# Kernel optimization log

Hardware: AMD Instinct MI355X
Metric: run time of the kernel (lower is better)

Reference implementation:

```python
import jax, jax.numpy as jnp
import numpy as np

N_CLASSES = 18
NMS_PRE = 1000   # test_cfg.nms_pre, per level
K_NMS = 500      # per-class candidates entering greedy NMS
SCORE_THR = 0.01
IOU_THR = 0.5
LEVEL_NS = [600000, 300000, 150000, 75000]


def _decode(points, pred):
    # fcaf3d axis-aligned decode: pred = (dx-, dx+, dy-, dy+, dz-, dz+) >= 0
    cx = points[:, 0] + (pred[:, 1] - pred[:, 0]) / 2
    cy = points[:, 1] + (pred[:, 3] - pred[:, 2]) / 2
    cz = points[:, 2] + (pred[:, 5] - pred[:, 4]) / 2
    w = pred[:, 0] + pred[:, 1]
    l = pred[:, 2] + pred[:, 3]
    h = pred[:, 4] + pred[:, 5]
    return jnp.stack([cx, cy, cz, w, l, h], axis=-1)  # [N, 6]


def _iou3d(b):
    # axis-aligned 3D IoU, b: [K,6] (cx,cy,cz,w,l,h) -> [K,K]
    mn = b[:, :3] - b[:, 3:] / 2
    mx = b[:, :3] + b[:, 3:] / 2
    lt = jnp.maximum(mn[:, None, :], mn[None, :, :])
    rb = jnp.minimum(mx[:, None, :], mx[None, :, :])
    inter = jnp.clip(rb - lt, 0.0).prod(-1)
    vol = jnp.clip(mx - mn, 0.0).prod(-1)
    return inter / (vol[:, None] + vol[None, :] - inter + 1e-6)


def _level(centerness, bbox_pred, cls_score, points):
    # fused score: cls.sigmoid() * centerness.sigmoid()
    scores = jax.nn.sigmoid(cls_score) * jax.nn.sigmoid(centerness)  # [N,C]
    max_scores = scores.max(axis=1)
    _, ids = jax.lax.top_k(max_scores, NMS_PRE)  # per-level prefilter
    bboxes = _decode(points[ids], bbox_pred[ids])  # [NMS_PRE, 6]
    return bboxes, scores[ids]


def _nms_class(boxes, scores):
    # boxes [M,6], scores [M] for one class -> greedy NMS on top K_NMS
    valid = scores > SCORE_THR
    s = jnp.where(valid, scores, -1.0)
    sv, order = jax.lax.top_k(s, K_NMS)  # sorted desc
    b = boxes[order]
    v = sv > SCORE_THR
    iou = _iou3d(b)  # [K,K]
    idx = jnp.arange(K_NMS)

    def body(i, sup):
        alive = jnp.logical_not(sup[i])
        return sup | (alive & (iou[i] > IOU_THR) & (idx > i))

    sup = jax.lax.fori_loop(0, K_NMS, body, jnp.logical_not(v))
    keep = jnp.logical_not(sup) & v
    return b, sv, keep


def _forward(levels):
    mlvl_bboxes, mlvl_scores = [], []
    for (cn, bp, cs, pt) in levels:
        b, s = _level(cn, bp, cs, pt)
        mlvl_bboxes.append(b)
        mlvl_scores.append(s)
    bboxes = jnp.concatenate(mlvl_bboxes)  # [4*NMS_PRE, 6]
    scores = jnp.concatenate(mlvl_scores)  # [4*NMS_PRE, C]
    # per-class NMS (vmap over class dim)
    b, sv, keep = jax.vmap(_nms_class, in_axes=(None, 1))(bboxes, scores)
    labels = jnp.broadcast_to(jnp.arange(N_CLASSES, dtype=jnp.int32)[:, None], sv.shape)
    return (b.reshape(-1, 6), sv.reshape(-1), labels.reshape(-1), keep.reshape(-1))


def setup_inputs() -> dict:
    key = jax.random.key(0)
    out = {}
    for li, n in enumerate(LEVEL_NS):
        k1, k2, k3, k4, key = jax.random.split(key, 5)
        out[f'centerness{li}'] = jax.random.normal(k1, (n, 1), jnp.float32)
        out[f'bbox_pred{li}'] = jax.random.uniform(k2, (n, 6), jnp.float32)  # non-negative distances
        out[f'cls_score{li}'] = jax.random.normal(k3, (n, N_CLASSES), jnp.float32)
        out[f'points{li}'] = jax.random.normal(k4, (n, 3), jnp.float32) * 2.0
    return out


def reference(centerness0, bbox_pred0, cls_score0, points0,
              centerness1, bbox_pred1, cls_score1, points1,
              centerness2, bbox_pred2, cls_score2, points2,
              centerness3, bbox_pred3, cls_score3, points3):
    levels = [
        (centerness0, bbox_pred0, cls_score0, points0),
        (centerness1, bbox_pred1, cls_score1, points1),
        (centerness2, bbox_pred2, cls_score2, points2),
        (centerness3, bbox_pred3, cls_score3, points3),
    ]
    return _forward(levels)
```

## Files before the change

kernel.cpp:

```cpp
#include <hip/hip_runtime.h>
#include <math.h>

#define N_CLASSES 18
#define NMS_PRE   1000
#define K_NMS     500
#define POOL      4000
#define LIST_CAP  2048
#define IOU_THR   0.5f
#define SCORE_THR 0.01f

typedef unsigned long long ull;

struct Ptrs {
  const float* cent[4];
  const float* bbox[4];
  const float* cls[4];
  const float* pts[4];
  int off[4];
  int ntot;
};

__device__ __forceinline__ unsigned int fsort(float f){
  unsigned int b = __float_as_uint(f);
  return (b & 0x80000000u) ? ~b : (b | 0x80000000u);
}
__device__ __forceinline__ float fsort_inv(unsigned int k){
  unsigned int b = (k & 0x80000000u) ? (k & 0x7FFFFFFFu) : ~k;
  return __uint_as_float(b);
}
__device__ __forceinline__ float sigmoidf_(float x){
  return 1.0f / (1.0f + expf(-x));
}
__device__ __forceinline__ int level_of(int f, const Ptrs& P){
  return (f >= P.off[3]) ? 3 : (f >= P.off[2]) ? 2 : (f >= P.off[1]) ? 1 : 0;
}

__device__ __forceinline__ void gload_lds16(const void* g, void* l){
  __builtin_amdgcn_global_load_lds(
      (const __attribute__((address_space(1))) void*)g,
      (__attribute__((address_space(3))) void*)l, 16, 0, 0);
}

__device__ __forceinline__ ull cx_keep(ull mine, ull part, bool keep_hi){
  ull mx = mine > part ? mine : part;
  ull mn = mine > part ? part : mine;
  return keep_hi ? mx : mn;
}
__device__ __forceinline__ void cxpair(ull &a, ull &b, bool a_hi){
  ull mx = a > b ? a : b;
  ull mn = a > b ? b : a;
  a = a_hi ? mx : mn;
  b = a_hi ? mn : mx;
}

__global__ void __launch_bounds__(256) init_kernel(unsigned int* hist, unsigned int* state,
                        unsigned int* cnts){
  for (int j = threadIdx.x; j < 4*2048; j += 256) hist[j] = 0u;
  if (threadIdx.x < 4){
    state[2*threadIdx.x]   = 0u;
    state[2*threadIdx.x+1] = NMS_PRE;
    cnts[threadIdx.x]      = 0u;
  }
}

__global__ void __launch_bounds__(256) compute_keys(Ptrs P, unsigned int* keys,
                        unsigned int* hist){
  __shared__ __align__(16) float cls_s[256*N_CLASSES];
  __shared__ unsigned int lh[2048];
  int t = threadIdx.x;
  int f0 = blockIdx.x << 8;
  int f = f0 + t;
  bool valid = f < P.ntot;
  int fl = min(f0 + 255, P.ntot - 1);
  bool uni = (level_of(f0, P) == level_of(fl, P)) && (f0 + 255 < P.ntot);
  int Lb = level_of(f0, P);

  if (uni){
    const float4* base4 = (const float4*)(P.cls[Lb] + (size_t)(f0 - P.off[Lb]) * N_CLASSES);
#pragma unroll
    for (int k = 0; k < 4; ++k){
      int j = (k << 8) + t;
      gload_lds16(base4 + j, (char*)cls_s + (size_t)j * 16);
    }
    if (t < 128){
      int j = 1024 + t;
      gload_lds16(base4 + j, (char*)cls_s + (size_t)j * 16);
    }
  }
  for (int j = t; j < 2048; j += 256) lh[j] = 0u;
  float m = 0.f, cent = 0.f;
  if (uni){
    cent = P.cent[Lb][f - P.off[Lb]];
  } else if (valid){
    int L = level_of(f, P); int i = f - P.off[L];
    const float* cl = P.cls[L] + (size_t)i * N_CLASSES;
    m = cl[0];
    for (int c = 1; c < N_CLASSES; ++c) m = fmaxf(m, cl[c]);
    cent = P.cent[L][i];
  }
  __syncthreads();

  if (uni){
    const float2* row = (const float2*)(cls_s + t * N_CLASSES);
    float2 v0 = row[0];
    m = fmaxf(v0.x, v0.y);
#pragma unroll
    for (int q = 1; q < 9; ++q){
      float2 v = row[q];
      m = fmaxf(m, fmaxf(v.x, v.y));
    }
  }
  if (valid){
    float s = sigmoidf_(m) * sigmoidf_(cent);
    unsigned int key = fsort(s);
    keys[f] = key;
    unsigned int bin = key >> 21;
    if (uni) atomicAdd(&lh[bin], 1u);
    else     atomicAdd(&hist[level_of(f, P)*2048 + bin], 1u);
  }
  __syncthreads();
  if (uni){
    for (int j = t; j < 2048; j += 256){
      unsigned int v = lh[j];
      if (v) atomicAdd(&hist[Lb*2048 + j], v);
    }
  }
}

__global__ void __launch_bounds__(256) hist_level(Ptrs P, const unsigned int* keys,
                        const unsigned int* state, unsigned int* hist){
  int f = blockIdx.x * 256 + threadIdx.x;
  if (f < P.ntot){
    int L = level_of(f, P);
    unsigned int key = keys[f];
    unsigned int Pfx = state[2*L];
    if ((key >> 21) == (Pfx >> 21))
      atomicAdd(&hist[L*2048 + ((key >> 10) & 0x7FFu)], 1u);
  }
}

__global__ void __launch_bounds__(256) scan_level(unsigned int* hist, unsigned int* state, int pass){
  __shared__ unsigned int lhist[4*2048];
  int t = threadIdx.x;
  int w = t >> 6, lane = t & 63;
  for (int j = t; j < 4*2048; j += 256) lhist[j] = hist[j];
  __syncthreads();
  {
    unsigned int krem = state[2*w + 1];
    unsigned int Pfx  = state[2*w];
    unsigned int carry = 0;
    for (int ch = 0; ch < 32; ++ch){
      int d = ch*64 + lane;
      unsigned int cnt = lhist[w*2048 + (2047 - d)];
      unsigned int pfx = cnt;
#pragma unroll
      for (int off = 1; off < 64; off <<= 1){
        unsigned int u = __shfl_up(pfx, off);
        if (lane >= off) pfx += u;
      }
      unsigned int C = carry + pfx;
      ull bal = __ballot(C >= krem);
      if (bal){
        int fl2 = __ffsll(bal) - 1;
        unsigned int Cf = __shfl(C, fl2);
        unsigned int cf = __shfl(cnt, fl2);
        if (lane == 0){
          unsigned int b = (unsigned int)(2047 - (ch*64 + fl2));
          state[2*w]     = (pass == 0) ? (b << 21) : (Pfx | (b << 10));
          state[2*w + 1] = krem - (Cf - cf);
        }
        break;
      }
      carry = __shfl(C, 63);
    }
  }
  if (pass == 0){
    __syncthreads();
    for (int j = t; j < 4*2048; j += 256) hist[j] = 0u;
  }
}

__global__ void __launch_bounds__(256) compact_kernel(Ptrs P, const unsigned int* keys,
                        const unsigned int* state, unsigned int* cnts, ull* lists){
  int f = blockIdx.x * 256 + threadIdx.x;
  if (f >= P.ntot) return;
  int L = level_of(f, P);
  unsigned int key = keys[f];
  unsigned int T = state[2*L];
  if (key >= T){
    unsigned int pos = atomicAdd(&cnts[L], 1u);
    if (pos < LIST_CAP){
      unsigned int i = (unsigned int)(f - P.off[L]);
      lists[(size_t)L*LIST_CAP + pos] = ((ull)key << 32) | (ull)(~i);
    }
  }
}

__global__ void __launch_bounds__(1024) sort_idx(const ull* lists,
                        const unsigned int* cnts, unsigned int* sidx){
  __shared__ ull buf[LIST_CAP];
  int L = blockIdx.x;
  int t = threadIdx.x;
  unsigned int cnt = cnts[L]; if (cnt > LIST_CAP) cnt = LIST_CAP;
  const ull* src = lists + (size_t)L*LIST_CAP;
  if (cnt <= 1024u){
    ull v0 = (t < (int)cnt) ? src[t] : 0ull;
    for (int k = 2; k <= 1024; k <<= 1){
      for (int j = k >> 1; j > 0; j >>= 1){
        bool hi0 = (((t & j) == 0) == ((t & k) == 0));
        if (j >= 64){
          __syncthreads();
          buf[t] = v0;
          __syncthreads();
          ull p0 = buf[t ^ j];
          v0 = cx_keep(v0, p0, hi0);
        } else {
          ull p0 = __shfl_xor(v0, j);
          v0 = cx_keep(v0, p0, hi0);
        }
      }
    }
    if (t < NMS_PRE) sidx[L*NMS_PRE + t] = ~((unsigned int)(v0 & 0xFFFFFFFFu));
  } else {
    int e1 = t + 1024;
    ull v0 = (t  < (int)cnt) ? src[t]  : 0ull;
    ull v1 = (e1 < (int)cnt) ? src[e1] : 0ull;
    for (int k = 2; k <= 2048; k <<= 1){
      for (int j = k >> 1; j > 0; j >>= 1){
        bool hi0 = (((t  & j) == 0) == ((t  & k) == 0));
        bool hi1 = (((e1 & j) == 0) == ((e1 & k) == 0));
        if (j >= 1024){
          cxpair(v0, v1, hi0);
        } else if (j >= 64){
          __syncthreads();
          buf[t] = v0; buf[e1] = v1;
          __syncthreads();
          ull p0 = buf[t ^ j];
          ull p1 = buf[e1 ^ j];
          v0 = cx_keep(v0, p0, hi0);
          v1 = cx_keep(v1, p1, hi1);
        } else {
          ull p0 = __shfl_xor(v0, j);
          ull p1 = __shfl_xor(v1, j);
          v0 = cx_keep(v0, p0, hi0);
          v1 = cx_keep(v1, p1, hi1);
        }
      }
    }
    if (t < NMS_PRE) sidx[L*NMS_PRE + t] = ~((unsigned int)(v0 & 0xFFFFFFFFu));
  }
}

__global__ void __launch_bounds__(64) gather_decode(Ptrs P, const unsigned int* sidx,
                        float* boxes_pool, float* scores_pool){
  int r = blockIdx.x*64 + threadIdx.x;
  if (r >= POOL) return;
  int L = r / NMS_PRE;
  unsigned int i = sidx[r];
  const float* bp = P.bbox[L] + (size_t)i * 6;
  const float* pp = P.pts[L]  + (size_t)i * 3;
  float p0 = bp[0], p1 = bp[1], p2 = bp[2], p3 = bp[3], p4 = bp[4], p5 = bp[5];
  float cx = pp[0] + (p1 - p0) * 0.5f;
  float cy = pp[1] + (p3 - p2) * 0.5f;
  float cz = pp[2] + (p5 - p4) * 0.5f;
  float w = p0 + p1, l = p2 + p3, h = p4 + p5;
  float* bo = boxes_pool + (size_t)r * 6;
  bo[0] = cx; bo[1] = cy; bo[2] = cz; bo[3] = w; bo[4] = l; bo[5] = h;
  float cs = sigmoidf_(P.cent[L][i]);
  const float* cl = P.cls[L] + (size_t)i * N_CLASSES;
#pragma unroll
  for (int c = 0; c < N_CLASSES; ++c)
    scores_pool[(size_t)c * POOL + r] = sigmoidf_(cl[c]) * cs;
}

__global__ void __launch_bounds__(1024) class_topk(const float* scores_pool, const float* boxes_pool,
                        float* out, float* aabb){
  __shared__ unsigned int keyS[4096];
  __shared__ ull comp[512];
  __shared__ unsigned int histS[256];
  __shared__ unsigned int wsum[16], wpre[16];
  __shared__ unsigned int sP, sK, sCnt;
  int c = blockIdx.x;
  int t = threadIdx.x;
  int w = t >> 6, lane = t & 63;

  for (int j = t; j < 4096; j += 1024){
    unsigned int k = 0u;
    if (j < POOL){
      float s = scores_pool[(size_t)c*POOL + j];
      float sval = (s > SCORE_THR) ? s : -1.0f;
      k = fsort(sval);
    }
    keyS[j] = k;
  }
  if (t == 0){ sP = 0u; sK = K_NMS; sCnt = 0u; }
  __syncthreads();

  for (int pass = 0; pass < 4; ++pass){
    int shift = 24 - 8*pass;
    if (t < 256) histS[t] = 0u;
    __syncthreads();
    unsigned int Pfx = sP;
    for (int j = t; j < 4096; j += 1024){
      unsigned int k = keyS[j];
      if ((((ull)(k ^ Pfx)) >> (shift + 8)) == 0ull)
        atomicAdd(&histS[(k >> shift) & 0xFFu], 1u);
    }
    __syncthreads();
    if (w == 0){
      unsigned int krem = sK;
      unsigned int carry = 0;
      for (int ch = 0; ch < 4; ++ch){
        unsigned int cnt = histS[255 - (ch*64 + lane)];
        unsigned int pfx = cnt;
#pragma unroll
        for (int off = 1; off < 64; off <<= 1){
          unsigned int u = __shfl_up(pfx, off);
          if (lane >= off) pfx += u;
        }
        unsigned int C = carry + pfx;
        ull bal = __ballot(C >= krem);
        if (bal){
          int fl = __ffsll(bal) - 1;
          unsigned int Cf = __shfl(C, fl);
          unsigned int cf = __shfl(cnt, fl);
          if (lane == 0){
            sP = Pfx | ((unsigned int)(255 - (ch*64 + fl)) << shift);
            sK = krem - (Cf - cf);
          }
          break;
        }
        carry = __shfl(C, 63);
      }
    }
    __syncthreads();
  }
  unsigned int T = sP, need = sK;

  unsigned int loc[4]; unsigned int ct = 0;
#pragma unroll
  for (int q = 0; q < 4; ++q){
    unsigned int k = keyS[4*t + q];
    loc[q] = k;
    ct += (k == T) ? 1u : 0u;
  }
  unsigned int inc = ct;
#pragma unroll
  for (int off = 1; off < 64; off <<= 1){
    unsigned int u = __shfl_up(inc, off);
    if (lane >= off) inc += u;
  }
  if (lane == 63) wsum[w] = inc;
  __syncthreads();
  if (t < 16){
    unsigned int v = wsum[t];
    unsigned int pincl = v;
#pragma unroll
    for (int off = 1; off < 16; off <<= 1){
      unsigned int u = __shfl_up(pincl, off);
      if (t >= off) pincl += u;
    }
    wpre[t] = pincl - v;
  }
  __syncthreads();
  unsigned int excl = wpre[w] + (inc - ct);

#pragma unroll
  for (int q = 0; q < 4; ++q){
    unsigned int k = loc[q];
    bool surv = false;
    if (k > T) surv = true;
    else if (k == T){ surv = (excl < need); excl += 1u; }
    if (surv){
      unsigned int pos = atomicAdd(&sCnt, 1u);
      if (pos < 512)
        comp[pos] = ((ull)k << 32) | (ull)(~(unsigned int)(4*t + q));
    }
  }
  __syncthreads();

  ull v0 = 0ull;
  if (t < 512 && t < (int)sCnt) v0 = comp[t];
  for (int k = 2; k <= 512; k <<= 1){
    for (int j = k >> 1; j > 0; j >>= 1){
      if (j >= 64){
        __syncthreads();
        if (t < 512) comp[t] = v0;
        __syncthreads();
        if (t < 512){
          ull p0 = comp[t ^ j];
          bool hi0 = (((t & j) == 0) == ((t & k) == 0));
          v0 = cx_keep(v0, p0, hi0);
        }
      } else {
        if (t < 512){
          ull p0 = __shfl_xor(v0, j);
          bool hi0 = (((t & j) == 0) == ((t & k) == 0));
          v0 = cx_keep(v0, p0, hi0);
        }
      }
    }
  }

  if (t < K_NMS){
    ull cm = v0;
    unsigned int j = ~((unsigned int)(cm & 0xFFFFFFFFu));
    float sval = fsort_inv((unsigned int)(cm >> 32));
    int o = c*K_NMS + t;
    const float* bp = boxes_pool + (size_t)j * 6;
    float b0 = bp[0], b1 = bp[1], b2 = bp[2], b3 = bp[3], b4 = bp[4], b5 = bp[5];
    float* ob = out + (size_t)o * 6;
    ob[0] = b0; ob[1] = b1; ob[2] = b2; ob[3] = b3; ob[4] = b4; ob[5] = b5;
    out[54000 + o] = sval;
    out[63000 + o] = (float)c;
    float mn0 = b0 - b3*0.5f, mx0 = b0 + b3*0.5f;
    float mn1 = b1 - b4*0.5f, mx1 = b1 + b4*0.5f;
    float mn2 = b2 - b5*0.5f, mx2 = b2 + b5*0.5f;
    float vol = fmaxf(mx0 - mn0, 0.f) * fmaxf(mx1 - mn1, 0.f) * fmaxf(mx2 - mn2, 0.f);
    float* ap = aabb + ((size_t)c*512 + t) * 8;
    ap[0] = mn0; ap[1] = mn1; ap[2] = mn2; ap[3] = mx0; ap[4] = mx1; ap[5] = mx2;
    ap[6] = vol; ap[7] = sval;
  }
}

__global__ void __launch_bounds__(512) nms_mask(const float* aabb, ull* maskG, ull* flagsG){
  __shared__ float smn0[512], smn1[512], smn2[512];
  __shared__ float smx0[512], smx1[512], smx2[512];
  __shared__ float svol[512];
  __shared__ ull rowbuf[64*8];
  int c = blockIdx.y, chunk = blockIdx.x;
  int t = threadIdx.x, w = t >> 6, lane = t & 63;
  float mn0 = 0.f, mn1 = 0.f, mn2 = 0.f, mx0 = 0.f, mx1 = 0.f, mx2 = 0.f, vol = 0.f;
  if (t < K_NMS){
    const float* ap = aabb + ((size_t)c*512 + t) * 8;
    mn0 = ap[0]; mn1 = ap[1]; mn2 = ap[2];
    mx0 = ap[3]; mx1 = ap[4]; mx2 = ap[5]; vol = ap[6];
  }
  smn0[t] = mn0; smn1[t] = mn1; smn2[t] = mn2;
  smx0[t] = mx0; smx1[t] = mx1; smx2[t] = mx2;
  svol[t] = vol;
  __syncthreads();
  int i0 = chunk * 64, i1 = min(i0 + 64, K_NMS);
  for (int i = i0; i < i1; ++i){
    float lt0 = fmaxf(smn0[i], mn0), lt1 = fmaxf(smn1[i], mn1), lt2 = fmaxf(smn2[i], mn2);
    float rb0 = fminf(smx0[i], mx0), rb1 = fminf(smx1[i], mx1), rb2 = fminf(smx2[i], mx2);
    float inter = fmaxf(rb0 - lt0, 0.f) * fmaxf(rb1 - lt1, 0.f) * fmaxf(rb2 - lt2, 0.f);
    float denom = svol[i] + vol - inter + 1e-6f;
    bool s = (t < K_NMS) && (t > i) && (inter / denom > IOU_THR);
    ull m = __ballot(s);
    if (lane == 0){
      maskG[((size_t)c*K_NMS + i)*8 + w] = m;
      rowbuf[(i - i0)*8 + w] = m;
    }
  }
  __syncthreads();
  if (t < 64){
    int r = i0 + t;
    bool nz = false;
    if (r < K_NMS){
      ull o = 0ull;
#pragma unroll
      for (int z = 0; z < 8; ++z) o |= rowbuf[t*8 + z];
      nz = (o != 0ull);
    }
    ull bal = __ballot(nz);
    if (t == 0) flagsG[(size_t)c*8 + chunk] = bal;
  }
}

__global__ void __launch_bounds__(512) nms_greedy(const float* aabb, const ull* maskG,
                        const ull* flagsG, float* keep_out){
  __shared__ ull maskS[K_NMS*8];
  __shared__ ull vbitsS[8], remS[8];
  int c = blockIdx.x, t = threadIdx.x, w = t >> 6, lane = t & 63;
  ull flg[8];
#pragma unroll
  for (int q = 0; q < 8; ++q) flg[q] = flagsG[(size_t)c*8 + q];
  for (int j = t; j < K_NMS*8; j += 512) maskS[j] = maskG[(size_t)c*K_NMS*8 + j];
  float sv = (t < K_NMS) ? aabb[((size_t)c*512 + t)*8 + 7] : -1.0f;
  ull vb = __ballot(sv > SCORE_THR);
  if (lane == 0) vbitsS[w] = vb;
  __syncthreads();
  if (w == 0){
    ull rem[8];
#pragma unroll
    for (int q = 0; q < 8; ++q) rem[q] = ~vbitsS[q];
#pragma unroll
    for (int q = 0; q < 8; ++q){
      ull cand = flg[q] & ~rem[q];
      while (cand){
        int b = __ffsll(cand) - 1;
        int i = q*64 + b;
#pragma unroll
        for (int z = 0; z < 8; ++z) rem[z] |= maskS[i*8 + z];
        ull above = (b < 63) ? (~0ull << (b + 1)) : 0ull;
        cand = flg[q] & ~rem[q] & above;
      }
    }
    if (lane == 0){
#pragma unroll
      for (int q = 0; q < 8; ++q) remS[q] = rem[q];
    }
  }
  __syncthreads();
  if (t < K_NMS)
    keep_out[c*K_NMS + t] = ((remS[t >> 6] >> (t & 63)) & 1ull) ? 0.0f : 1.0f;
}

extern "C" void kernel_launch(void* const* d_in, const int* in_sizes, int n_in,
                              void* d_out, int out_size, void* d_ws, size_t ws_size,
                              hipStream_t stream){
  Ptrs P;
  int off = 0;
  for (int L = 0; L < 4; ++L){
    P.cent[L] = (const float*)d_in[4*L + 0];
    P.bbox[L] = (const float*)d_in[4*L + 1];
    P.cls[L]  = (const float*)d_in[4*L + 2];
    P.pts[L]  = (const float*)d_in[4*L + 3];
    P.off[L]  = off;
    off += in_sizes[4*L + 0];
  }
  P.ntot = off;

  char* w = (char*)d_ws;
  size_t o = 0;
  auto alloc = [&](size_t bytes) -> char* {
    char* p = w + o;
    o = (o + bytes + 255) & ~(size_t)255;
    return p;
  };
  unsigned int* keys        = (unsigned int*)alloc((size_t)P.ntot * 4);
  unsigned int* hist        = (unsigned int*)alloc(4 * 2048 * 4);
  unsigned int* state       = (unsigned int*)alloc(4 * 2 * 4);
  unsigned int* cnts        = (unsigned int*)alloc(4 * 4);
  ull* lists                = (ull*)alloc((size_t)4 * LIST_CAP * 8);
  unsigned int* sidx        = (unsigned int*)alloc((size_t)POOL * 4);
  float* boxes_pool         = (float*)alloc((size_t)POOL * 6 * 4);
  float* scores_pool        = (float*)alloc((size_t)N_CLASSES * POOL * 4);
  float* aabb               = (float*)alloc((size_t)N_CLASSES * 512 * 8 * 4);
  ull* maskG                = (ull*)alloc((size_t)N_CLASSES * K_NMS * 8 * 8);
  ull* flagsG               = (ull*)alloc((size_t)N_CLASSES * 8 * 8);

  float* out = (float*)d_out;
  int grid = (P.ntot + 255) / 256;

  init_kernel<<<1, 256, 0, stream>>>(hist, state, cnts);
  compute_keys<<<grid, 256, 0, stream>>>(P, keys, hist);
  scan_level<<<1, 256, 0, stream>>>(hist, state, 0);
  hist_level<<<grid, 256, 0, stream>>>(P, keys, state, hist);
  scan_level<<<1, 256, 0, stream>>>(hist, state, 1);
  compact_kernel<<<grid, 256, 0, stream>>>(P, keys, state, cnts, lists);
  sort_idx<<<4, 1024, 0, stream>>>(lists, cnts, sidx);
  gather_decode<<<(POOL + 63)/64, 64, 0, stream>>>(P, sidx, boxes_pool, scores_pool);
  class_topk<<<N_CLASSES, 1024, 0, stream>>>(scores_pool, boxes_pool, out, aabb);
  nms_mask<<<dim3(8, N_CLASSES), 512, 0, stream>>>(aabb, maskG, flagsG);
  nms_greedy<<<N_CLASSES, 512, 0, stream>>>(aabb, maskG, flagsG, out + 72000);
}
```

Before: 302.1 us.

## Replicate histograms and shard compaction counters to reduce global atomic contention

The first-pass radix histogram is replicated across 16 copies indexed by block, and scan_sel sums the copies, with one block per level instead of a single block. Compaction uses 16 padded sub-counters per level writing into fixed sub-slots of a zero-initialised list, so the sort always runs the 2048-element path. The aim is to cut same-address global atomic contention in the hot full-grid kernels. In exchange there is more init work, always sorting 2048 elements, and a risk of dropping candidates if one sub-list overflows its 128 slots.

```diff
diff --git a/kernel.cpp b/kernel.cpp
--- a/kernel.cpp
+++ b/kernel.cpp
@@ -6,6 +6,9 @@
 #define K_NMS     500
 #define POOL      4000
 #define LIST_CAP  2048
+#define NREP      16
+#define NSUB      16
+#define SUBCAP    (LIST_CAP/NSUB)
 #define IOU_THR   0.5f
 #define SCORE_THR 0.01f
 
@@ -53,23 +56,28 @@
   b = a_hi ? mn : mx;
 }
 
-__global__ void __launch_bounds__(256) init_kernel(unsigned int* hist, unsigned int* state,
-                        unsigned int* cnts){
-  for (int j = threadIdx.x; j < 4*2048; j += 256) hist[j] = 0u;
-  if (threadIdx.x < 4){
-    state[2*threadIdx.x]   = 0u;
-    state[2*threadIdx.x+1] = NMS_PRE;
-    cnts[threadIdx.x]      = 0u;
+__global__ void __launch_bounds__(256) init_kernel(unsigned int* hist_rep, unsigned int* hist2,
+                        unsigned int* scnt, ull* lists, unsigned int* state){
+  int tid = blockIdx.x*256 + threadIdx.x;
+  int stride = gridDim.x*256;
+  for (int j = tid; j < NREP*4*2048; j += stride) hist_rep[j] = 0u;
+  for (int j = tid; j < 4*2048; j += stride) hist2[j] = 0u;
+  for (int j = tid; j < 4*NSUB*16; j += stride) scnt[j] = 0u;
+  for (int j = tid; j < 4*LIST_CAP; j += stride) lists[j] = 0ull;
+  if (tid < 4){
+    state[2*tid]   = 0u;
+    state[2*tid+1] = NMS_PRE;
   }
 }
 
 __global__ void __launch_bounds__(256) compute_keys(Ptrs P, unsigned int* keys,
-                        unsigned int* hist){
+                        unsigned int* hist_rep){
   __shared__ __align__(16) float cls_s[256*N_CLASSES];
   __shared__ unsigned int lh[2048];
   int t = threadIdx.x;
   int f0 = blockIdx.x << 8;
   int f = f0 + t;
+  int rep = blockIdx.x & (NREP - 1);
   bool valid = f < P.ntot;
   int fl = min(f0 + 255, P.ntot - 1);
   bool uni = (level_of(f0, P) == level_of(fl, P)) && (f0 + 255 < P.ntot);
@@ -116,42 +124,47 @@
     keys[f] = key;
     unsigned int bin = key >> 21;
     if (uni) atomicAdd(&lh[bin], 1u);
-    else     atomicAdd(&hist[level_of(f, P)*2048 + bin], 1u);
+    else     atomicAdd(&hist_rep[((rep*4) + level_of(f, P))*2048 + bin], 1u);
   }
   __syncthreads();
   if (uni){
+    unsigned int* hb = hist_rep + ((rep*4) + Lb)*2048;
     for (int j = t; j < 2048; j += 256){
       unsigned int v = lh[j];
-      if (v) atomicAdd(&hist[Lb*2048 + j], v);
+      if (v) atomicAdd(&hb[j], v);
     }
   }
 }
 
 __global__ void __launch_bounds__(256) hist_level(Ptrs P, const unsigned int* keys,
-                        const unsigned int* state, unsigned int* hist){
+                        const unsigned int* state, unsigned int* hist2){
   int f = blockIdx.x * 256 + threadIdx.x;
   if (f < P.ntot){
     int L = level_of(f, P);
     unsigned int key = keys[f];
     unsigned int Pfx = state[2*L];
     if ((key >> 21) == (Pfx >> 21))
-      atomicAdd(&hist[L*2048 + ((key >> 10) & 0x7FFu)], 1u);
-  }
-}
-
-__global__ void __launch_bounds__(256) scan_level(unsigned int* hist, unsigned int* state, int pass){
-  __shared__ unsigned int lhist[4*2048];
-  int t = threadIdx.x;
-  int w = t >> 6, lane = t & 63;
-  for (int j = t; j < 4*2048; j += 256) lhist[j] = hist[j];
-  __syncthreads();
-  {
-    unsigned int krem = state[2*w + 1];
-    unsigned int Pfx  = state[2*w];
+      atomicAdd(&hist2[L*2048 + ((key >> 10) & 0x7FFu)], 1u);
+  }
+}
+
+__global__ void __launch_bounds__(512) scan_sel(const unsigned int* src, int nrep,
+                        unsigned int* state, int pass){
+  __shared__ unsigned int lhist[2048];
+  int L = blockIdx.x, t = threadIdx.x;
+  for (int j = t; j < 2048; j += 512){
+    unsigned int s = 0u;
+    for (int r = 0; r < nrep; ++r) s += src[((r*4) + L)*2048 + j];
+    lhist[j] = s;
+  }
+  __syncthreads();
+  if (t < 64){
+    int lane = t;
+    unsigned int krem = state[2*L + 1];
+    unsigned int Pfx  = state[2*L];
     unsigned int carry = 0;
     for (int ch = 0; ch < 32; ++ch){
-      int d = ch*64 + lane;
-      unsigned int cnt = lhist[w*2048 + (2047 - d)];
+      unsigned int cnt = lhist[2047 - (ch*64 + lane)];
       unsigned int pfx = cnt;
 #pragma unroll
       for (int off = 1; off < 64; off <<= 1){
@@ -166,89 +179,64 @@
         unsigned int cf = __shfl(cnt, fl2);
         if (lane == 0){
           unsigned int b = (unsigned int)(2047 - (ch*64 + fl2));
-          state[2*w]     = (pass == 0) ? (b << 21) : (Pfx | (b << 10));
-          state[2*w + 1] = krem - (Cf - cf);
+          state[2*L]     = (pass == 0) ? (b << 21) : (Pfx | (b << 10));
+          state[2*L + 1] = krem - (Cf - cf);
         }
         break;
       }
       carry = __shfl(C, 63);
     }
   }
-  if (pass == 0){
-    __syncthreads();
-    for (int j = t; j < 4*2048; j += 256) hist[j] = 0u;
-  }
 }
 
 __global__ void __launch_bounds__(256) compact_kernel(Ptrs P, const unsigned int* keys,
-                        const unsigned int* state, unsigned int* cnts, ull* lists){
+                        const unsigned int* state, unsigned int* scnt, ull* lists){
   int f = blockIdx.x * 256 + threadIdx.x;
   if (f >= P.ntot) return;
   int L = level_of(f, P);
   unsigned int key = keys[f];
   unsigned int T = state[2*L];
   if (key >= T){
-    unsigned int pos = atomicAdd(&cnts[L], 1u);
-    if (pos < LIST_CAP){
+    unsigned int sub = (unsigned int)blockIdx.x & (NSUB - 1);
+    unsigned int pos = atomicAdd(&scnt[(L*NSUB + sub)*16], 1u);
+    if (pos < SUBCAP){
       unsigned int i = (unsigned int)(f - P.off[L]);
-      lists[(size_t)L*LIST_CAP + pos] = ((ull)key << 32) | (ull)(~i);
-    }
-  }
-}
-
-__global__ void __launch_bounds__(1024) sort_idx(const ull* lists,
-                        const unsigned int* cnts, unsigned int* sidx){
+      lists[(size_t)L*LIST_CAP + sub*SUBCAP + pos] = ((ull)key << 32) | (ull)(~i);
+    }
+  }
+}
+
+__global__ void __launch_bounds__(1024) sort_idx(const ull* lists, unsigned int* sidx){
   __shared__ ull buf[LIST_CAP];
   int L = blockIdx.x;
   int t = threadIdx.x;
-  unsigned int cnt = cnts[L]; if (cnt > LIST_CAP) cnt = LIST_CAP;
+  int e1 = t + 1024;
   const ull* src = lists + (size_t)L*LIST_CAP;
-  if (cnt <= 1024u){
-    ull v0 = (t < (int)cnt) ? src[t] : 0ull;
-    for (int k = 2; k <= 1024; k <<= 1){
-      for (int j = k >> 1; j > 0; j >>= 1){
-        bool hi0 = (((t & j) == 0) == ((t & k) == 0));
-        if (j >= 64){
-          __syncthreads();
-          buf[t] = v0;
-          __syncthreads();
-          ull p0 = buf[t ^ j];
-          v0 = cx_keep(v0, p0, hi0);
-        } else {
-          ull p0 = __shfl_xor(v0, j);
-          v0 = cx_keep(v0, p0, hi0);
-        }
+  ull v0 = src[t];
+  ull v1 = src[e1];
+  for (int k = 2; k <= 2048; k <<= 1){
+    for (int j = k >> 1; j > 0; j >>= 1){
+      bool hi0 = (((t  & j) == 0) == ((t  & k) == 0));
+      bool hi1 = (((e1 & j) == 0) == ((e1 & k) == 0));
+      if (j >= 1024){
+        cxpair(v0, v1, hi0);
+      } else if (j >= 64){
+        __syncthreads();
+        buf[t] = v0; buf[e1] = v1;
+        __syncthreads();
+        ull p0 = buf[t ^ j];
+        ull p1 = buf[e1 ^ j];
+        v0 = cx_keep(v0, p0, hi0);
+        v1 = cx_keep(v1, p1, hi1);
+      } else {
+        ull p0 = __shfl_xor(v0, j);
+        ull p1 = __shfl_xor(v1, j);
+        v0 = cx_keep(v0, p0, hi0);
+        v1 = cx_keep(v1, p1, hi1);
       }
     }
-    if (t < NMS_PRE) sidx[L*NMS_PRE + t] = ~((unsigned int)(v0 & 0xFFFFFFFFu));
-  } else {
-    int e1 = t + 1024;
-    ull v0 = (t  < (int)cnt) ? src[t]  : 0ull;
-    ull v1 = (e1 < (int)cnt) ? src[e1] : 0ull;
-    for (int k = 2; k <= 2048; k <<= 1){
-      for (int j = k >> 1; j > 0; j >>= 1){
-        bool hi0 = (((t  & j) == 0) == ((t  & k) == 0));
-        bool hi1 = (((e1 & j) == 0) == ((e1 & k) == 0));
-        if (j >= 1024){
-          cxpair(v0, v1, hi0);
-        } else if (j >= 64){
-          __syncthreads();
-          buf[t] = v0; buf[e1] = v1;
-          __syncthreads();
-          ull p0 = buf[t ^ j];
-          ull p1 = buf[e1 ^ j];
-          v0 = cx_keep(v0, p0, hi0);
-          v1 = cx_keep(v1, p1, hi1);
-        } else {
-          ull p0 = __shfl_xor(v0, j);
-          ull p1 = __shfl_xor(v1, j);
-          v0 = cx_keep(v0, p0, hi0);
-          v1 = cx_keep(v1, p1, hi1);
-        }
-      }
-    }
-    if (t < NMS_PRE) sidx[L*NMS_PRE + t] = ~((unsigned int)(v0 & 0xFFFFFFFFu));
-  }
+  }
+  if (t < NMS_PRE) sidx[L*NMS_PRE + t] = ~((unsigned int)(v0 & 0xFFFFFFFFu));
 }
 
 __global__ void __launch_bounds__(64) gather_decode(Ptrs P, const unsigned int* sidx,
@@ -530,9 +518,10 @@
     return p;
   };
   unsigned int* keys        = (unsigned int*)alloc((size_t)P.ntot * 4);
-  unsigned int* hist        = (unsigned int*)alloc(4 * 2048 * 4);
+  unsigned int* hist_rep    = (unsigned int*)alloc((size_t)NREP * 4 * 2048 * 4);
+  unsigned int* hist2       = (unsigned int*)alloc(4 * 2048 * 4);
   unsigned int* state       = (unsigned int*)alloc(4 * 2 * 4);
-  unsigned int* cnts        = (unsigned int*)alloc(4 * 4);
+  unsigned int* scnt        = (unsigned int*)alloc(4 * NSUB * 16 * 4);
   ull* lists                = (ull*)alloc((size_t)4 * LIST_CAP * 8);
   unsigned int* sidx        = (unsigned int*)alloc((size_t)POOL * 4);
   float* boxes_pool         = (float*)alloc((size_t)POOL * 6 * 4);
@@ -544,13 +533,13 @@
   float* out = (float*)d_out;
   int grid = (P.ntot + 255) / 256;
 
-  init_kernel<<<1, 256, 0, stream>>>(hist, state, cnts);
-  compute_keys<<<grid, 256, 0, stream>>>(P, keys, hist);
-  scan_level<<<1, 256, 0, stream>>>(hist, state, 0);
-  hist_level<<<grid, 256, 0, stream>>>(P, keys, state, hist);
-  scan_level<<<1, 256, 0, stream>>>(hist, state, 1);
-  compact_kernel<<<grid, 256, 0, stream>>>(P, keys, state, cnts, lists);
-  sort_idx<<<4, 1024, 0, stream>>>(lists, cnts, sidx);
+  init_kernel<<<64, 256, 0, stream>>>(hist_rep, hist2, scnt, lists, state);
+  compute_keys<<<grid, 256, 0, stream>>>(P, keys, hist_rep);
+  scan_sel<<<4, 512, 0, stream>>>(hist_rep, NREP, state, 0);
+  hist_level<<<grid, 256, 0, stream>>>(P, keys, state, hist2);
+  scan_sel<<<4, 512, 0, stream>>>(hist2, 1, state, 1);
+  compact_kernel<<<grid, 256, 0, stream>>>(P, keys, state, scnt, lists);
+  sort_idx<<<4, 1024, 0, stream>>>(lists, sidx);
   gather_decode<<<(POOL + 63)/64, 64, 0, stream>>>(P, sidx, boxes_pool, scores_pool);
   class_topk<<<N_CLASSES, 1024, 0, stream>>>(scores_pool, boxes_pool, out, aabb);
   nms_mask<<<dim3(8, N_CLASSES), 512, 0, stream>>>(aabb, maskG, flagsG);
```

New measurement: 266.2 us. -11.9%, faster.
